# Kernel optimization log

Measured on AMD Instinct MI355X. Metric: run time of the kernel, lower is better.

## Reference

```python
import jax, jax.numpy as jnp
from jax import lax
import numpy as np

B, N0 = 4, 4096
NIN, NH, NOUT = 16, 128, 2
DEPTH, K, RADIUS, KNN = 3, 64, 2.0, 3
EPS = 1e-5


def _bn(x, g, b):
    # eval-mode BatchNorm1d with running_mean=0, running_var=1
    return g * x / jnp.sqrt(1.0 + EPS) + b


def _mlp2(h, p):
    # Seq(Lin, ReLU, BN) x 2, as in MLP([d, d, out])
    w1, b1, g1, be1, w2, b2, g2, be2 = p
    h = _bn(jax.nn.relu(h @ w1 + b1), g1, be1)
    return _bn(jax.nn.relu(h @ w2 + b2), g2, be2)


def _fps(pts, m):
    # farthest point sampling, deterministic start at index 0
    n = pts.shape[0]
    def step(carry, _):
        dmin, last = carry
        d = jnp.sum((pts - pts[last]) ** 2, axis=-1)
        dmin = jnp.minimum(dmin, d)
        nxt = jnp.argmax(dmin).astype(jnp.int32)
        return (dmin, nxt), nxt
    _, rest = lax.scan(step, (jnp.full((n,), 1e30, pts.dtype), jnp.int32(0)), None, length=m - 1)
    return jnp.concatenate([jnp.zeros((1,), jnp.int32), rest])


def _sa(xx, pp, m, params):
    # SAModule with PointConv: fps -> radius(K nearest within r) -> gather-MLP-max
    idx = _fps(pp, m)
    q = pp[idx]                                              # [m,3] sampled centers
    d2 = jnp.sum((q[:, None, :] - pp[None, :, :]) ** 2, -1)  # [m,n]
    d2 = jnp.where(d2 <= RADIUS * RADIUS, d2, 1e30)
    neg, nbr = lax.top_k(-d2, K)                             # K nearest inside ball
    valid = neg > -1e29
    h = jnp.concatenate([xx[nbr], pp[nbr] - q[:, None, :]], axis=-1)  # [m,K,C+3]
    h = _mlp2(h, params)
    h = jnp.where(valid[..., None], h, -1e30)
    return jnp.max(h, axis=1), q                             # PointConv max aggr


def _fp(xx, pp, xs, ps, params):
    # FPModule: knn_interpolate (k=3, inverse squared-distance weights) + concat skip + MLP
    d2 = jnp.sum((ps[:, None, :] - pp[None, :, :]) ** 2, -1)  # [n_fine, n_coarse]
    neg, idx = lax.top_k(-d2, KNN)
    w = 1.0 / jnp.maximum(-neg, 1e-16)
    y = jnp.sum(w[..., None] * xx[idx], axis=1) / jnp.sum(w, axis=1, keepdims=True)
    return _mlp2(jnp.concatenate([y, xs], axis=-1), params)


def _forward(x, pos, lin_in_w, lin_in_b,
             sa_w1, sa_b1, sa_g1, sa_be1, sa_w2, sa_b2, sa_g2, sa_be2,
             fp_w1, fp_b1, fp_g1, fp_be1, fp_w2, fp_b2, fp_g2, fp_be2,
             lo_w1, lo_b1, lo_g1, lo_be1, lo_w2, lo_b2, lo_g2, lo_be2):
    xb = jax.nn.relu(x.reshape(B, N0, NIN) @ lin_in_w + lin_in_b)  # lin_in + ReLU
    posb = pos.reshape(B, N0, 3)
    sa = [(xb, posb)]
    n = N0
    for i in range(DEPTH):
        m = n // 2  # ratio = 0.5
        p = (sa_w1[i], sa_b1[i], sa_g1[i], sa_be1[i], sa_w2[i], sa_b2[i], sa_g2[i], sa_be2[i])
        h, q = jax.vmap(lambda a, b: _sa(a, b, m, p))(sa[i][0], sa[i][1])
        sa.append((h, q))
        n = m
    xf, posf = sa[DEPTH]
    for step in range(DEPTH):
        mi = DEPTH - 1 - step
        xs, ps = sa[DEPTH - 1 - step]
        p = (fp_w1[mi], fp_b1[mi], fp_g1[mi], fp_be1[mi], fp_w2[mi], fp_b2[mi], fp_g2[mi], fp_be2[mi])
        xf = jax.vmap(lambda a, b, c, d: _fp(a, b, c, d, p))(xf, posf, xs, ps)
        posf = ps
    out = _mlp2(xf, (lo_w1, lo_b1, lo_g1, lo_be1, lo_w2, lo_b2, lo_g2, lo_be2))
    return out.reshape(B * N0, NOUT)


def setup_inputs() -> dict:
    key = jax.random.key(0)
    ki = iter(jax.random.split(key, 24))
    def nrm(shape, s=0.1):
        return jax.random.normal(next(ki), shape, jnp.float32) * s
    D = NH + 3   # PointConv MLP in-dim
    F = 2 * NH   # FP MLP in-dim (nIn + nSkip)
    return {
        "x": jax.random.normal(next(ki), (B * N0, NIN), jnp.float32),
        "pos": jax.random.uniform(next(ki), (B * N0, 3), jnp.float32) * 16.0,
        "batch": jnp.repeat(jnp.arange(B, dtype=jnp.int32), N0),
        "lin_in_w": nrm((NIN, NH)), "lin_in_b": nrm((NH,)),
        "sa_w1": nrm((DEPTH, D, D)), "sa_b1": nrm((DEPTH, D)),
        "sa_g1": jnp.ones((DEPTH, D)), "sa_be1": jnp.zeros((DEPTH, D)),
        "sa_w2": nrm((DEPTH, D, NH)), "sa_b2": nrm((DEPTH, NH)),
        "sa_g2": jnp.ones((DEPTH, NH)), "sa_be2": jnp.zeros((DEPTH, NH)),
        "fp_w1": nrm((DEPTH, F, F)), "fp_b1": nrm((DEPTH, F)),
        "fp_g1": jnp.ones((DEPTH, F)), "fp_be1": jnp.zeros((DEPTH, F)),
        "fp_w2": nrm((DEPTH, F, NH)), "fp_b2": nrm((DEPTH, NH)),
        "fp_g2": jnp.ones((DEPTH, NH)), "fp_be2": jnp.zeros((DEPTH, NH)),
        "lo_w1": nrm((NH, NH)), "lo_b1": nrm((NH,)),
        "lo_g1": jnp.ones((NH,)), "lo_be1": jnp.zeros((NH,)),
        "lo_w2": nrm((NH, NOUT)), "lo_b2": nrm((NOUT,)),
        "lo_g2": jnp.ones((NOUT,)), "lo_be2": jnp.zeros((NOUT,)),
    }


def reference(x, pos, batch, lin_in_w, lin_in_b,
              sa_w1, sa_b1, sa_g1, sa_be1, sa_w2, sa_b2, sa_g2, sa_be2,
              fp_w1, fp_b1, fp_g1, fp_be1, fp_w2, fp_b2, fp_g2, fp_be2,
              lo_w1, lo_b1, lo_g1, lo_be1, lo_w2, lo_b2, lo_g2, lo_be2):
    return _forward(x, pos, lin_in_w, lin_in_b,
                    sa_w1, sa_b1, sa_g1, sa_be1, sa_w2, sa_b2, sa_g2, sa_be2,
                    fp_w1, fp_b1, fp_g1, fp_be1, fp_w2, fp_b2, fp_g2, fp_be2,
                    lo_w1, lo_b1, lo_g1, lo_be1, lo_w2, lo_b2, lo_g2, lo_be2)
```

## Files before the change

### kernel.cpp

```cpp
#include <hip/hip_runtime.h>
#include <cstddef>


#define EPSF 1e-5f

typedef __attribute__((ext_vector_type(2))) float f32x2;

__device__ __forceinline__ f32x2 f2splat(float s) {
    f32x2 v; v.x = s; v.y = s; return v;
}

__device__ __forceinline__ float d2_rn(float dx, float dy, float dz) {
    return __fadd_rn(__fadd_rn(__fmul_rn(dx, dx), __fmul_rn(dy, dy)), __fmul_rn(dz, dz));
}

template <int CTRL, int RMASK>
__device__ __forceinline__ float dpp_max_f32(float v) {
    int o = __builtin_amdgcn_update_dpp(__float_as_int(v), __float_as_int(v),
                                        CTRL, RMASK, 0xf, false);
    return fmaxf(v, __int_as_float(o));
}

template <int N, int NT>
__device__ void fps_role(const float* __restrict__ pts, float* __restrict__ q,
                         const int m, const int b, char* smem) {
#pragma clang fp contract(off)
    constexpr int PPT = N / NT;
    constexpr int PH = PPT / 2;
    constexpr int NW = NT / 64;
    float* s_px = (float*)smem;
    float* s_py = s_px + N;
    float* s_pz = s_py + N;
    int*   s_qi = (int*)(s_pz + N);
    float2* s_slot = (float2*)(s_qi + N / 2);
    const int t = threadIdx.x;
    const int wave = t >> 6, lane = t & 63;
    const int base = t * PPT;
    const float* P = pts + (size_t)b * N * 3;
    asm volatile("s_setprio 3");
    f32x2 rx[PH], ry[PH], rz[PH], dmin[PH];
#pragma unroll
    for (int j = 0; j < PH; ++j) {
        int i = base + 2 * j;
        float x0 = P[i * 3 + 0], y0 = P[i * 3 + 1], z0 = P[i * 3 + 2];
        float x1 = P[i * 3 + 3], y1 = P[i * 3 + 4], z1 = P[i * 3 + 5];
        rx[j].x = x0; rx[j].y = x1;
        ry[j].x = y0; ry[j].y = y1;
        rz[j].x = z0; rz[j].y = z1;
        dmin[j] = f2splat(1e30f);
        s_px[i] = x0; s_px[i + 1] = x1;
        s_py[i] = y0; s_py[i + 1] = y1;
        s_pz[i] = z0; s_pz[i + 1] = z1;
    }
    float lx = P[0], ly = P[1], lz = P[2];
    if (t == 0) s_qi[0] = 0;

    for (int step = 1; step < m; ++step) {
        float bv = -1.0f; int bj = 0;
        const f32x2 lxv = f2splat(lx), lyv = f2splat(ly), lzv = f2splat(lz);
#pragma unroll
        for (int j = 0; j < PH; ++j) {
            f32x2 dx = rx[j] - lxv;
            f32x2 dy = ry[j] - lyv;
            f32x2 dz = rz[j] - lzv;
            f32x2 d = dx * dx + dy * dy + dz * dz;
            float m0 = fminf(dmin[j].x, d.x);
            float m1 = fminf(dmin[j].y, d.y);
            dmin[j].x = m0; dmin[j].y = m1;
            if (m0 > bv) { bv = m0; bj = 2 * j; }
            if (m1 > bv) { bv = m1; bj = 2 * j + 1; }
        }
        const int bidx = base + bj;

        float v = bv;
        v = dpp_max_f32<0x111, 0xf>(v);
        v = dpp_max_f32<0x112, 0xf>(v);
        v = dpp_max_f32<0x114, 0xf>(v);
        v = dpp_max_f32<0x118, 0xf>(v);
        v = dpp_max_f32<0x142, 0xa>(v);
        v = dpp_max_f32<0x143, 0xc>(v);
        const float mv = __int_as_float(__builtin_amdgcn_readlane(__float_as_int(v), 63));
        unsigned long long mb = __ballot(bv == mv);
        const int wl = __ffsll((long long)mb) - 1;
        const int wbi = __builtin_amdgcn_readlane(bidx, wl);

        const int p = step & 1;
        if (lane == 0) s_slot[p * NW + wave] = make_float2(mv, __int_as_float(wbi));
        __syncthreads();

        float2 sl = s_slot[p * NW + (lane & (NW - 1))];
        float gvt = sl.x;
        gvt = dpp_max_f32<0x111, 0xf>(gvt);
        gvt = dpp_max_f32<0x112, 0xf>(gvt);
        if (NW == 8) gvt = dpp_max_f32<0x114, 0xf>(gvt);
        const float gm = __int_as_float(
            __builtin_amdgcn_readlane(__float_as_int(gvt), NW - 1));
        unsigned long long gb = __ballot((lane < NW) && (sl.x == gm));
        const int gl = __ffsll((long long)gb) - 1;
        const int gi = __builtin_amdgcn_readlane(__float_as_int(sl.y), gl);

        lx = s_px[gi]; ly = s_py[gi]; lz = s_pz[gi];
        if (t == 0) s_qi[step] = gi;
    }
    __syncthreads();
    for (int e = t; e < m; e += NT) {
        int gi = s_qi[e];
        size_t o = ((size_t)b * m + e) * 3;
        q[o] = s_px[gi]; q[o + 1] = s_py[gi]; q[o + 2] = s_pz[gi];
    }
}

__device__ void lin_role(const float* __restrict__ x, const float* __restrict__ w,
                         const float* __restrict__ bias, float* __restrict__ xb,
                         const int blk) {
    const int t = threadIdx.x;
    const int row = blk * 2 + (t >> 7);
    const int col = t & 127;
    float acc = bias[col];
#pragma unroll
    for (int k = 0; k < 16; ++k) acc = fmaf(x[row * 16 + k], w[k * 128 + col], acc);
    xb[row * 128 + col] = fmaxf(acc, 0.0f);
}

template <int CHUNK, int WACT>
__device__ void nbr_role(const float* __restrict__ pts, const float* __restrict__ q,
                         int2* __restrict__ pairs, unsigned* __restrict__ counter,
                         const int n, const int m, const int pstr, const int qstr,
                         const int blk, char* smem) {
    const int w = threadIdx.x >> 6, lane = threadIdx.x & 63;
    if (w >= WACT) return;
    float* D = (float*)smem + w * CHUNK * 64;
    const int c = blk * WACT + w;
    const int b = c / m;
    const int r = c - b * m;
    const float* P = pts + (size_t)b * pstr * 3;
    const size_t qo = ((size_t)b * qstr + r) * 3;
    const float qx = q[qo + 0];
    const float qy = q[qo + 1];
    const float qz = q[qo + 2];
    for (int s = 0; s < CHUNK; ++s) {
        int i = s * 64 + lane;
        float d2 = d2_rn(P[i * 3] - qx, P[i * 3 + 1] - qy, P[i * 3 + 2] - qz);
        D[i] = (d2 <= 4.0f) ? d2 : 1e30f;
    }
    int my_g = -1;
    int cnt = 0;
    for (int round = 0; round < 64; ++round) {
        float bv = 3e38f;
        int bi = 0x7fffffff;
        for (int s = 0; s < CHUNK; ++s) {
            int i = s * 64 + lane;
            float v = D[i];
            if (v < bv) { bv = v; bi = i; }
        }
#pragma unroll
        for (int off = 32; off >= 1; off >>= 1) {
            float ov = __shfl_xor(bv, off, 64);
            int   oi = __shfl_xor(bi, off, 64);
            if (ov < bv || (ov == bv && oi < bi)) { bv = ov; bi = oi; }
        }
        if (bv > 1e29f) break;
        if (round == lane) my_g = bi;
        if (lane == (bi & 63)) D[bi] = 3e38f;
        ++cnt;
    }
    unsigned base = 0;
    if (lane == 0) base = atomicAdd(counter, (unsigned)cnt);
    base = (unsigned)__shfl((int)base, 0, 64);
    if (lane < cnt) pairs[base + lane] = make_int2(c, my_g);
}

typedef float Row132[132];
__device__ void sa_body(const float* __restrict__ xx, const float* __restrict__ ptsc,
    const float* __restrict__ qc, const int2* __restrict__ pairs,
    const unsigned* __restrict__ vcount,
    const float* __restrict__ wp1, const float* __restrict__ b1,
    const float* __restrict__ g1, const float* __restrict__ be1,
    const float* __restrict__ wp2, const float* __restrict__ b2,
    const float* __restrict__ g2, const float* __restrict__ be2,
    float* __restrict__ hout, const int lm, const int ln, const int lnp,
    const int blk, char* smem) {
    Row132* shA = (Row132*)smem;
    int* sh_c = (int*)(smem + 33792);
    int* sh_g = sh_c + 64;
    const int t = threadIdx.x;
    const int V = (int)*vcount;
    const int r0 = blk * 64;
    if (r0 >= V) return;
    if (t < 64) {
        int r = r0 + t;
        if (r < V) { int2 p = pairs[r]; sh_c[t] = p.x; sh_g[t] = p.y; }
        else { sh_c[t] = -1; sh_g[t] = 0; }
    }
    __syncthreads();

    for (int e = t; e < 64 * 33; e += 256) {
        int row = e / 33, cid = e - row * 33;
        int c = sh_c[row];
        float4 v = make_float4(0.f, 0.f, 0.f, 0.f);
        if (c >= 0) {
            int g = sh_g[row];
            int b = c >> lm;
            if (cid < 32) {
                size_t ptf = ((size_t)(b << ln) + g);
                v = *(const float4*)(xx + (ptf << 7) + cid * 4);
            } else {
                size_t ptc = ((size_t)(b << lnp) + g);
                const float* P = ptsc + ptc * 3;
                int r = c - (b << lm);
                const float* Q = qc + ((size_t)((b << 11) + r)) * 3;
                v.x = P[0] - Q[0]; v.y = P[1] - Q[1]; v.z = P[2] - Q[2]; v.w = 0.f;
            }
        }
        *(float4*)&shA[row][cid * 4] = v;
    }
    __syncthreads();

    const float invs = 1.0f / sqrtf(1.0f + EPSF);
    const int tr = t >> 4, tc = t & 15;
    const int xrow = t >> 2, xcol = t & 3;
    float acc[32];
#pragma unroll
    for (int i = 0; i < 32; ++i) acc[i] = 0.0f;
    float accx = 0.0f;

    for (int k = 0; k < 132; k += 4) {
        const float4 A0 = *(const float4*)&shA[tr     ][k];
        const float4 A1 = *(const float4*)&shA[tr + 16][k];
        const float4 A2 = *(const float4*)&shA[tr + 32][k];
        const float4 A3 = *(const float4*)&shA[tr + 48][k];
        const float4 AX = *(const float4*)&shA[xrow][k];
        const float a0v[4] = {A0.x, A0.y, A0.z, A0.w};
        const float a1v[4] = {A1.x, A1.y, A1.z, A1.w};
        const float a2v[4] = {A2.x, A2.y, A2.z, A2.w};
        const float a3v[4] = {A3.x, A3.y, A3.z, A3.w};
        const float axv[4] = {AX.x, AX.y, AX.z, AX.w};
#pragma unroll
        for (int u = 0; u < 4; ++u) {
            const float* wr = wp1 + (size_t)(k + u) * 132;
            const float4 w0 = *(const float4*)(wr + 8 * tc);
            const float4 w1v = *(const float4*)(wr + 8 * tc + 4);
            const float wx = wr[128 + xcol];
            const float wa[8] = {w0.x, w0.y, w0.z, w0.w, w1v.x, w1v.y, w1v.z, w1v.w};
#pragma unroll
            for (int j = 0; j < 8; ++j) {
                acc[0 * 8 + j] = fmaf(a0v[u], wa[j], acc[0 * 8 + j]);
                acc[1 * 8 + j] = fmaf(a1v[u], wa[j], acc[1 * 8 + j]);
                acc[2 * 8 + j] = fmaf(a2v[u], wa[j], acc[2 * 8 + j]);
                acc[3 * 8 + j] = fmaf(a3v[u], wa[j], acc[3 * 8 + j]);
            }
            accx = fmaf(axv[u], wx, accx);
        }
    }
    __syncthreads();
#pragma unroll
    for (int i = 0; i < 4; ++i)
#pragma unroll
        for (int j = 0; j < 8; ++j) {
            int col = 8 * tc + j;
            float z = fmaxf(acc[i * 8 + j] + b1[col], 0.0f);
            shA[tr + 16 * i][col] = g1[col] * z * invs + be1[col];
        }
    if (xcol < 3) {
        int col = 128 + xcol;
        float z = fmaxf(accx + b1[col], 0.0f);
        shA[xrow][col] = g1[col] * z * invs + be1[col];
    } else {
        shA[xrow][131] = 0.0f;
    }
    __syncthreads();

#pragma unroll
    for (int i = 0; i < 32; ++i) acc[i] = 0.0f;
    for (int k = 0; k < 132; k += 4) {
        const float4 A0 = *(const float4*)&shA[tr     ][k];
        const float4 A1 = *(const float4*)&shA[tr + 16][k];
        const float4 A2 = *(const float4*)&shA[tr + 32][k];
        const float4 A3 = *(const float4*)&shA[tr + 48][k];
        const float a0v[4] = {A0.x, A0.y, A0.z, A0.w};
        const float a1v[4] = {A1.x, A1.y, A1.z, A1.w};
        const float a2v[4] = {A2.x, A2.y, A2.z, A2.w};
        const float a3v[4] = {A3.x, A3.y, A3.z, A3.w};
#pragma unroll
        for (int u = 0; u < 4; ++u) {
            const float* wr = wp2 + (size_t)(k + u) * 128;
            const float4 w0 = *(const float4*)(wr + 8 * tc);
            const float4 w1v = *(const float4*)(wr + 8 * tc + 4);
            const float wa[8] = {w0.x, w0.y, w0.z, w0.w, w1v.x, w1v.y, w1v.z, w1v.w};
#pragma unroll
            for (int j = 0; j < 8; ++j) {
                acc[0 * 8 + j] = fmaf(a0v[u], wa[j], acc[0 * 8 + j]);
                acc[1 * 8 + j] = fmaf(a1v[u], wa[j], acc[1 * 8 + j]);
                acc[2 * 8 + j] = fmaf(a2v[u], wa[j], acc[2 * 8 + j]);
                acc[3 * 8 + j] = fmaf(a3v[u], wa[j], acc[3 * 8 + j]);
            }
        }
    }
    __syncthreads();
#pragma unroll
    for (int i = 0; i < 4; ++i)
#pragma unroll
        for (int j = 0; j < 8; ++j) {
            int col = 8 * tc + j;
            float z = fmaxf(acc[i * 8 + j] + b2[col], 0.0f);
            shA[tr + 16 * i][col] = g2[col] * z * invs + be2[col];
        }
    __syncthreads();

    if (t < 128) {
        const int col = t;
        float run = -1.0f;
        int cur = sh_c[0];
        for (int row = 0; row < 64; ++row) {
            int c = sh_c[row];
            if (c != cur) {
                if (cur >= 0)
                    atomicMax((unsigned*)&hout[((size_t)cur << 7) + col], __float_as_uint(run));
                run = -1.0f; cur = c;
            }
            run = fmaxf(run, shA[row][col]);
        }
        if (cur >= 0)
            atomicMax((unsigned*)&hout[((size_t)cur << 7) + col], __float_as_uint(run));
    }
}

__device__ void knn_role(const float* __restrict__ pf, const float* __restrict__ pc,
                         int* __restrict__ kidx, float* __restrict__ kw,
                         const int nf, const int nc, const int fstr, const int cstr,
                         const int blk) {
    const int tg = blk * 256 + threadIdx.x;
    const int b = tg / nf;
    const int rf = tg - b * nf;
    const float* F = pf + ((size_t)b * fstr + rf) * 3;
    const float fx = F[0], fy = F[1], fz = F[2];
    const float* C = pc + (size_t)b * cstr * 3;
    float b0 = 1e30f, b1 = 1e30f, b2 = 1e30f;
    int i0 = 0, i1 = 0, i2 = 0;
    for (int j = 0; j < nc; ++j) {
        float d2 = d2_rn(C[j * 3] - fx, C[j * 3 + 1] - fy, C[j * 3 + 2] - fz);
        if (d2 < b0)      { b2 = b1; i2 = i1; b1 = b0; i1 = i0; b0 = d2; i0 = j; }
        else if (d2 < b1) { b2 = b1; i2 = i1; b1 = d2; i1 = j; }
        else if (d2 < b2) { b2 = d2; i2 = j; }
    }
    float w0 = 1.0f / fmaxf(b0, 1e-16f);
    float w1 = 1.0f / fmaxf(b1, 1e-16f);
    float w2 = 1.0f / fmaxf(b2, 1e-16f);
    float inv = 1.0f / (w0 + w1 + w2);
    size_t o = (size_t)tg * 3;
    kidx[o] = i0; kidx[o + 1] = i1; kidx[o + 2] = i2;
    kw[o] = w0 * inv; kw[o + 1] = w1 * inv; kw[o + 2] = w2 * inv;
}

__global__ __launch_bounds__(256) void stage_a_kernel(
    const float* __restrict__ pos, float* __restrict__ q1,
    const float* __restrict__ x, const float* __restrict__ lin_w,
    const float* __restrict__ lin_b, float* __restrict__ xb,
    float* __restrict__ hbuf, unsigned* __restrict__ ctrs,
    const float* __restrict__ sa_w1, const float* __restrict__ sa_w2,
    float* __restrict__ wp1, float* __restrict__ wp2) {
    __shared__ __align__(16) char smem[57408];
    const int blk = blockIdx.x;
    if (blk < 4) {
        fps_role<4096, 256>(pos, q1, 2048, blk, smem);
    } else if (blk < 4 + 8192) {
        lin_role(x, lin_w, lin_b, xb, blk - 4);
    } else if (blk < 4 + 8192 + 1792) {
        const int i = blk - 8196;
        *(float4*)(hbuf + (size_t)i * 1024 + threadIdx.x * 4) =
            make_float4(0.f, 0.f, 0.f, 0.f);
        if (i == 0 && threadIdx.x < 3) ctrs[threadIdx.x * 16] = 0u;
    } else {
        const int f = (blk - 9988) * 256 + threadIdx.x;
        if (f < 52272) {
            int col = f % 132; int r = f / 132;
            int k = r % 132; int lvl = r / 132;
            float v = 0.0f;
            if (k < 131 && col < 131)
                v = sa_w1[(size_t)lvl * 131 * 131 + k * 131 + col];
            wp1[f] = v;
        } else if (f < 52272 + 50688) {
            int f2 = f - 52272;
            int col = f2 & 127; int r = f2 >> 7;
            int k = r % 132; int lvl = r / 132;
            float v = 0.0f;
            if (k < 131)
                v = sa_w2[(size_t)lvl * 131 * 128 + k * 128 + col];
            wp2[f2] = v;
        }
    }
}

__global__ __launch_bounds__(256) void stage_b_kernel(
    const float* __restrict__ pos, const float* __restrict__ q1,
    int2* __restrict__ pairs1, unsigned* __restrict__ ctr0,
    int2* __restrict__ pairs2, unsigned* __restrict__ ctr1,
    int2* __restrict__ pairs3, unsigned* __restrict__ ctr2,
    int* __restrict__ kidx2, float* __restrict__ kw2,
    int* __restrict__ kidx1, float* __restrict__ kw1,
    int* __restrict__ kidx0, float* __restrict__ kw0) {
    __shared__ __align__(16) char smem[32768];
    const int blk = blockIdx.x;
    if (blk < 4096)
        nbr_role<64, 2>(pos, q1, pairs1, ctr0, 4096, 2048, 4096, 2048, blk, smem);
    else if (blk < 4096 + 1024)
        nbr_role<32, 4>(q1, q1, pairs2, ctr1, 2048, 1024, 2048, 2048, blk - 4096, smem);
    else if (blk < 4096 + 1024 + 512)
        nbr_role<16, 4>(q1, q1, pairs3, ctr2, 1024, 512, 2048, 2048, blk - 5120, smem);
    else if (blk < 5632 + 64)
        knn_role(pos, q1, kidx2, kw2, 4096, 2048, 4096, 2048, blk - 5632);
    else if (blk < 5696 + 32)
        knn_role(q1, q1, kidx1, kw1, 2048, 1024, 2048, 2048, blk - 5696);
    else
        knn_role(q1, q1, kidx0, kw0, 1024, 512, 2048, 2048, blk - 5728);
}

__global__ __launch_bounds__(256) void sa_fused_kernel(
    const float* xx, const float* ptsc, const float* qc, const int2* pairs,
    const unsigned* vcount,
    const float* wp1, const float* b1, const float* g1, const float* be1,
    const float* wp2, const float* b2, const float* g2, const float* be2,
    float* hout, int lm, int ln, int lnp) {
    __shared__ __align__(16) char smem[34304];
    sa_body(xx, ptsc, qc, pairs, vcount, wp1, b1, g1, be1, wp2, b2, g2, be2,
            hout, lm, ln, lnp, blockIdx.x, smem);
}

__global__ __launch_bounds__(256) void fp_fused_kernel(
    const float* __restrict__ xc, const float* __restrict__ xs,
    const int* __restrict__ kidx, const float* __restrict__ kw,
    const float* __restrict__ w1, const float* __restrict__ b1,
    const float* __restrict__ g1, const float* __restrict__ be1,
    const float* __restrict__ w2, const float* __restrict__ b2,
    const float* __restrict__ g2, const float* __restrict__ be2,
    float* __restrict__ out, int lnf) {
    __shared__ __align__(16) float shA[32][260];
    const int t = threadIdx.x;
    const int r0 = blockIdx.x * 32;
    const float invs = 1.0f / sqrtf(1.0f + EPSF);

    for (int e = t; e < 32 * 64; e += 256) {
        int r = e >> 6, cid = e & 63;
        int fr = r0 + r;
        float4 v;
        if (cid < 32) {
            int b = fr >> lnf;
            size_t o = (size_t)fr * 3;
            int i0 = kidx[o], i1 = kidx[o + 1], i2 = kidx[o + 2];
            float u0 = kw[o], u1 = kw[o + 1], u2 = kw[o + 2];
            const float* X = xc + (((size_t)b << lnf) >> 1) * 128;
            const float4 A0 = *(const float4*)(X + (size_t)i0 * 128 + cid * 4);
            const float4 A1 = *(const float4*)(X + (size_t)i1 * 128 + cid * 4);
            const float4 A2 = *(const float4*)(X + (size_t)i2 * 128 + cid * 4);
            v.x = u0 * A0.x + u1 * A1.x + u2 * A2.x;
            v.y = u0 * A0.y + u1 * A1.y + u2 * A2.y;
            v.z = u0 * A0.z + u1 * A1.z + u2 * A2.z;
            v.w = u0 * A0.w + u1 * A1.w + u2 * A2.w;
        } else {
            v = *(const float4*)(xs + (size_t)fr * 128 + (cid - 32) * 4);
        }
        *(float4*)&shA[r][cid * 4] = v;
    }
    __syncthreads();

    const int tr = t >> 5, tc = t & 31;
    float acc[32];
#pragma unroll
    for (int i = 0; i < 32; ++i) acc[i] = 0.0f;
    for (int k = 0; k < 256; k += 4) {
        const float4 A0 = *(const float4*)&shA[tr     ][k];
        const float4 A1 = *(const float4*)&shA[tr +  8][k];
        const float4 A2 = *(const float4*)&shA[tr + 16][k];
        const float4 A3 = *(const float4*)&shA[tr + 24][k];
        const float a0v[4] = {A0.x, A0.y, A0.z, A0.w};
        const float a1v[4] = {A1.x, A1.y, A1.z, A1.w};
        const float a2v[4] = {A2.x, A2.y, A2.z, A2.w};
        const float a3v[4] = {A3.x, A3.y, A3.z, A3.w};
#pragma unroll
        for (int u = 0; u < 4; ++u) {
            const float* wr = w1 + (size_t)(k + u) * 256;
            const float4 w0v = *(const float4*)(wr + 8 * tc);
            const float4 w1v = *(const float4*)(wr + 8 * tc + 4);
            const float wa[8] = {w0v.x, w0v.y, w0v.z, w0v.w, w1v.x, w1v.y, w1v.z, w1v.w};
#pragma unroll
            for (int j = 0; j < 8; ++j) {
                acc[0 * 8 + j] = fmaf(a0v[u], wa[j], acc[0 * 8 + j]);
                acc[1 * 8 + j] = fmaf(a1v[u], wa[j], acc[1 * 8 + j]);
                acc[2 * 8 + j] = fmaf(a2v[u], wa[j], acc[2 * 8 + j]);
                acc[3 * 8 + j] = fmaf(a3v[u], wa[j], acc[3 * 8 + j]);
            }
        }
    }
    __syncthreads();
#pragma unroll
    for (int i = 0; i < 4; ++i)
#pragma unroll
        for (int j = 0; j < 8; ++j) {
            int col = 8 * tc + j;
            float z = fmaxf(acc[i * 8 + j] + b1[col], 0.0f);
            shA[tr + 8 * i][col] = g1[col] * z * invs + be1[col];
        }
    __syncthreads();

    const int tr2 = t >> 4, tc2 = t & 15;
    float acc2[16];
#pragma unroll
    for (int i = 0; i < 16; ++i) acc2[i] = 0.0f;
    for (int k = 0; k < 256; k += 4) {
        const float4 A0 = *(const float4*)&shA[tr2     ][k];
        const float4 A1 = *(const float4*)&shA[tr2 + 16][k];
        const float a0v[4] = {A0.x, A0.y, A0.z, A0.w};
        const float a1v[4] = {A1.x, A1.y, A1.z, A1.w};
#pragma unroll
        for (int u = 0; u < 4; ++u) {
            const float* wr = w2 + (size_t)(k + u) * 128;
            const float4 w0v = *(const float4*)(wr + 8 * tc2);
            const float4 w1v = *(const float4*)(wr + 8 * tc2 + 4);
            const float wa[8] = {w0v.x, w0v.y, w0v.z, w0v.w, w1v.x, w1v.y, w1v.z, w1v.w};
#pragma unroll
            for (int j = 0; j < 8; ++j) {
                acc2[0 * 8 + j] = fmaf(a0v[u], wa[j], acc2[0 * 8 + j]);
                acc2[1 * 8 + j] = fmaf(a1v[u], wa[j], acc2[1 * 8 + j]);
            }
        }
    }
#pragma unroll
    for (int i = 0; i < 2; ++i)
#pragma unroll
        for (int j = 0; j < 8; ++j) {
            int col = 8 * tc2 + j;
            int fr = r0 + tr2 + 16 * i;
            float z = fmaxf(acc2[i * 8 + j] + b2[col], 0.0f);
            out[(size_t)fr * 128 + col] = g2[col] * z * invs + be2[col];
        }
}

__global__ __launch_bounds__(256) void lo_fused_kernel(
    const float* __restrict__ in,
    const float* __restrict__ w1, const float* __restrict__ b1,
    const float* __restrict__ g1, const float* __restrict__ be1,
    const float* __restrict__ w2, const float* __restrict__ b2,
    const float* __restrict__ g2, const float* __restrict__ be2,
    float* __restrict__ out) {
    __shared__ __align__(16) float shA[32][132];
    const int t = threadIdx.x;
    const int r0 = blockIdx.x * 32;
    const float invs = 1.0f / sqrtf(1.0f + EPSF);

    for (int e = t; e < 32 * 32; e += 256) {
        int r = e >> 5, cid = e & 31;
        *(float4*)&shA[r][cid * 4] =
            *(const float4*)(in + (size_t)(r0 + r) * 128 + cid * 4);
    }
    __syncthreads();

    const int tr = t >> 4, tc = t & 15;
    float acc[16];
#pragma unroll
    for (int i = 0; i < 16; ++i) acc[i] = 0.0f;
    for (int k = 0; k < 128; k += 4) {
        const float4 A0 = *(const float4*)&shA[2 * tr + 0][k];
        const float4 A1 = *(const float4*)&shA[2 * tr + 1][k];
        const float a0v[4] = {A0.x, A0.y, A0.z, A0.w};
        const float a1v[4] = {A1.x, A1.y, A1.z, A1.w};
#pragma unroll
        for (int u = 0; u < 4; ++u) {
            const float* wr = w1 + (size_t)(k + u) * 128;
            const float4 w0v = *(const float4*)(wr + 8 * tc);
            const float4 w1v = *(const float4*)(wr + 8 * tc + 4);
            const float wa[8] = {w0v.x, w0v.y, w0v.z, w0v.w, w1v.x, w1v.y, w1v.z, w1v.w};
#pragma unroll
            for (int j = 0; j < 8; ++j) {
                acc[0 * 8 + j] = fmaf(a0v[u], wa[j], acc[0 * 8 + j]);
                acc[1 * 8 + j] = fmaf(a1v[u], wa[j], acc[1 * 8 + j]);
            }
        }
    }
    __syncthreads();
#pragma unroll
    for (int i = 0; i < 2; ++i)
#pragma unroll
        for (int j = 0; j < 8; ++j) {
            int col = 8 * tc + j;
            float z = fmaxf(acc[i * 8 + j] + b1[col], 0.0f);
            shA[2 * tr + i][col] = g1[col] * z * invs + be1[col];
        }
    __syncthreads();

    if (t < 64) {
        const int row = t >> 1, col = t & 1;
        float a = b2[col];
        for (int k = 0; k < 128; ++k)
            a = fmaf(shA[row][k], w2[k * 2 + col], a);
        a = fmaxf(a, 0.0f);
        out[(size_t)(r0 + row) * 2 + col] = g2[col] * a * invs + be2[col];
    }
}

extern "C" void kernel_launch(void* const* d_in, const int* in_sizes, int n_in,
                              void* d_out, int out_size, void* d_ws, size_t ws_size,
                              hipStream_t stream) {
    const float* x      = (const float*)d_in[0];
    const float* pos    = (const float*)d_in[1];
    const float* lin_w  = (const float*)d_in[3];
    const float* lin_b  = (const float*)d_in[4];
    const float* sa_w1  = (const float*)d_in[5];
    const float* sa_b1  = (const float*)d_in[6];
    const float* sa_g1  = (const float*)d_in[7];
    const float* sa_be1 = (const float*)d_in[8];
    const float* sa_w2  = (const float*)d_in[9];
    const float* sa_b2  = (const float*)d_in[10];
    const float* sa_g2  = (const float*)d_in[11];
    const float* sa_be2 = (const float*)d_in[12];
    const float* fp_w1  = (const float*)d_in[13];
    const float* fp_b1  = (const float*)d_in[14];
    const float* fp_g1  = (const float*)d_in[15];
    const float* fp_be1 = (const float*)d_in[16];
    const float* fp_w2  = (const float*)d_in[17];
    const float* fp_b2  = (const float*)d_in[18];
    const float* fp_g2  = (const float*)d_in[19];
    const float* fp_be2 = (const float*)d_in[20];
    const float* lo_w1  = (const float*)d_in[21];
    const float* lo_b1  = (const float*)d_in[22];
    const float* lo_g1  = (const float*)d_in[23];
    const float* lo_be1 = (const float*)d_in[24];
    const float* lo_w2  = (const float*)d_in[25];
    const float* lo_b2  = (const float*)d_in[26];
    const float* lo_g2  = (const float*)d_in[27];
    const float* lo_be2 = (const float*)d_in[28];

    float* ws = (float*)d_ws;
    size_t off = 0;
    auto alloc = [&](size_t n) { float* p = ws + off; off += n; return p; };
    float* xb    = alloc(4 * 4096 * 128);
    float* q1    = alloc(4 * 2048 * 3);
    float* h1    = alloc(4 * 2048 * 128);
    float* h2    = alloc(4 * 1024 * 128);
    float* h3    = alloc(4 * 512 * 128);
    int2* pairs1 = (int2*)alloc(4 * 2048 * 64 * 2);
    int2* pairs2 = (int2*)alloc(4 * 1024 * 64 * 2);
    int2* pairs3 = (int2*)alloc(4 * 512 * 64 * 2);
    unsigned* ctrs = (unsigned*)alloc(64);
    int* kidx0   = (int*)alloc(4 * 1024 * 3);
    float* kw0   = alloc(4 * 1024 * 3);
    int* kidx1   = (int*)alloc(4 * 2048 * 3);
    float* kw1   = alloc(4 * 2048 * 3);
    int* kidx2   = (int*)alloc(4 * 4096 * 3);
    float* kw2   = alloc(4 * 4096 * 3);
    float* xfA   = alloc(4 * 4096 * 128);
    float* xfB   = alloc(4 * 4096 * 128);
    float* wp1   = alloc(3 * 132 * 132);
    float* wp2   = alloc(3 * 132 * 128);
    if (ws_size < off * sizeof(float)) return;

    stage_a_kernel<<<4 + 8192 + 1792 + 403, 256, 0, stream>>>(
        pos, q1, x, lin_w, lin_b, xb, h1, ctrs, sa_w1, sa_w2, wp1, wp2);

    stage_b_kernel<<<4096 + 1024 + 512 + 64 + 32 + 16, 256, 0, stream>>>(
        pos, q1, pairs1, ctrs + 0, pairs2, ctrs + 16, pairs3, ctrs + 32,
        kidx2, kw2, kidx1, kw1, kidx0, kw0);

    sa_fused_kernel<<<8192, 256, 0, stream>>>(xb, pos, q1, pairs1, ctrs + 0,
        wp1, sa_b1, sa_g1, sa_be1, wp2, sa_b2, sa_g2, sa_be2,
        h1, 11, 12, 12);

    sa_fused_kernel<<<4096, 256, 0, stream>>>(h1, q1, q1, pairs2, ctrs + 16,
        wp1 + 132 * 132, sa_b1 + 131, sa_g1 + 131, sa_be1 + 131,
        wp2 + 132 * 128, sa_b2 + 128, sa_g2 + 128, sa_be2 + 128,
        h2, 10, 11, 11);

    sa_fused_kernel<<<2048, 256, 0, stream>>>(h2, q1, q1, pairs3, ctrs + 32,
        wp1 + 2 * 132 * 132, sa_b1 + 2 * 131, sa_g1 + 2 * 131, sa_be1 + 2 * 131,
        wp2 + 2 * 132 * 128, sa_b2 + 2 * 128, sa_g2 + 2 * 128, sa_be2 + 2 * 128,
        h3, 9, 10, 11);

    fp_fused_kernel<<<4 * 1024 / 32, 256, 0, stream>>>(h3, h2, kidx0, kw0,
        fp_w1 + 2 * 256 * 256, fp_b1 + 2 * 256, fp_g1 + 2 * 256, fp_be1 + 2 * 256,
        fp_w2 + 2 * 256 * 128, fp_b2 + 2 * 128, fp_g2 + 2 * 128, fp_be2 + 2 * 128,
        xfA, 10);

    fp_fused_kernel<<<4 * 2048 / 32, 256, 0, stream>>>(xfA, h1, kidx1, kw1,
        fp_w1 + 256 * 256, fp_b1 + 256, fp_g1 + 256, fp_be1 + 256,
        fp_w2 + 256 * 128, fp_b2 + 128, fp_g2 + 128, fp_be2 + 128,
        xfB, 11);

    fp_fused_kernel<<<4 * 4096 / 32, 256, 0, stream>>>(xfB, xb, kidx2, kw2,
        fp_w1, fp_b1, fp_g1, fp_be1, fp_w2, fp_b2, fp_g2, fp_be2,
        xfA, 12);

    lo_fused_kernel<<<16384 / 32, 256, 0, stream>>>(xfA,
        lo_w1, lo_b1, lo_g1, lo_be1, lo_w2, lo_b2, lo_g2, lo_be2,
        (float*)d_out);
}
```

Baseline: 2.699 ms.

## Remap SA MLP GEMM to per-wave column slices with wave-uniform weights

The SA fused kernel's two-layer MLP now gives each wave a contiguous slice of output columns (33 or 32) and each lane one gathered row, so weight reads are wave-uniform and can be broadcast or scalarised. Before, each thread computed a 4x8 tile and read per-lane weight vectors from global memory. The packed weight buffers are re-laid out per wave (36- and 32-wide slices) in the stage-A prep role to match. The cost is that every lane reads its own shared-memory row, which may cause bank conflicts, and it needs 33 accumulators with less register reuse of A.

Result: slower. 3.659 ms (+35.6%).

```diff
diff --git a/kernel.cpp b/kernel.cpp
--- a/kernel.cpp
+++ b/kernel.cpp
@@ -217,95 +217,88 @@
     __syncthreads();
 
     const float invs = 1.0f / sqrtf(1.0f + EPSF);
-    const int tr = t >> 4, tc = t & 15;
-    const int xrow = t >> 2, xcol = t & 3;
-    float acc[32];
-#pragma unroll
-    for (int i = 0; i < 32; ++i) acc[i] = 0.0f;
-    float accx = 0.0f;
-
-    for (int k = 0; k < 132; k += 4) {
-        const float4 A0 = *(const float4*)&shA[tr     ][k];
-        const float4 A1 = *(const float4*)&shA[tr + 16][k];
-        const float4 A2 = *(const float4*)&shA[tr + 32][k];
-        const float4 A3 = *(const float4*)&shA[tr + 48][k];
-        const float4 AX = *(const float4*)&shA[xrow][k];
-        const float a0v[4] = {A0.x, A0.y, A0.z, A0.w};
-        const float a1v[4] = {A1.x, A1.y, A1.z, A1.w};
-        const float a2v[4] = {A2.x, A2.y, A2.z, A2.w};
-        const float a3v[4] = {A3.x, A3.y, A3.z, A3.w};
-        const float axv[4] = {AX.x, AX.y, AX.z, AX.w};
-#pragma unroll
-        for (int u = 0; u < 4; ++u) {
-            const float* wr = wp1 + (size_t)(k + u) * 132;
-            const float4 w0 = *(const float4*)(wr + 8 * tc);
-            const float4 w1v = *(const float4*)(wr + 8 * tc + 4);
-            const float wx = wr[128 + xcol];
-            const float wa[8] = {w0.x, w0.y, w0.z, w0.w, w1v.x, w1v.y, w1v.z, w1v.w};
-#pragma unroll
-            for (int j = 0; j < 8; ++j) {
-                acc[0 * 8 + j] = fmaf(a0v[u], wa[j], acc[0 * 8 + j]);
-                acc[1 * 8 + j] = fmaf(a1v[u], wa[j], acc[1 * 8 + j]);
-                acc[2 * 8 + j] = fmaf(a2v[u], wa[j], acc[2 * 8 + j]);
-                acc[3 * 8 + j] = fmaf(a3v[u], wa[j], acc[3 * 8 + j]);
-            }
-            accx = fmaf(axv[u], wx, accx);
-        }
-    }
-    __syncthreads();
-#pragma unroll
-    for (int i = 0; i < 4; ++i)
-#pragma unroll
-        for (int j = 0; j < 8; ++j) {
-            int col = 8 * tc + j;
-            float z = fmaxf(acc[i * 8 + j] + b1[col], 0.0f);
-            shA[tr + 16 * i][col] = g1[col] * z * invs + be1[col];
-        }
-    if (xcol < 3) {
-        int col = 128 + xcol;
-        float z = fmaxf(accx + b1[col], 0.0f);
-        shA[xrow][col] = g1[col] * z * invs + be1[col];
-    } else {
-        shA[xrow][131] = 0.0f;
-    }
-    __syncthreads();
-
-#pragma unroll
-    for (int i = 0; i < 32; ++i) acc[i] = 0.0f;
-    for (int k = 0; k < 132; k += 4) {
-        const float4 A0 = *(const float4*)&shA[tr     ][k];
-        const float4 A1 = *(const float4*)&shA[tr + 16][k];
-        const float4 A2 = *(const float4*)&shA[tr + 32][k];
-        const float4 A3 = *(const float4*)&shA[tr + 48][k];
-        const float a0v[4] = {A0.x, A0.y, A0.z, A0.w};
-        const float a1v[4] = {A1.x, A1.y, A1.z, A1.w};
-        const float a2v[4] = {A2.x, A2.y, A2.z, A2.w};
-        const float a3v[4] = {A3.x, A3.y, A3.z, A3.w};
-#pragma unroll
-        for (int u = 0; u < 4; ++u) {
-            const float* wr = wp2 + (size_t)(k + u) * 128;
-            const float4 w0 = *(const float4*)(wr + 8 * tc);
-            const float4 w1v = *(const float4*)(wr + 8 * tc + 4);
-            const float wa[8] = {w0.x, w0.y, w0.z, w0.w, w1v.x, w1v.y, w1v.z, w1v.w};
-#pragma unroll
-            for (int j = 0; j < 8; ++j) {
-                acc[0 * 8 + j] = fmaf(a0v[u], wa[j], acc[0 * 8 + j]);
-                acc[1 * 8 + j] = fmaf(a1v[u], wa[j], acc[1 * 8 + j]);
-                acc[2 * 8 + j] = fmaf(a2v[u], wa[j], acc[2 * 8 + j]);
-                acc[3 * 8 + j] = fmaf(a3v[u], wa[j], acc[3 * 8 + j]);
-            }
-        }
-    }
-    __syncthreads();
-#pragma unroll
-    for (int i = 0; i < 4; ++i)
-#pragma unroll
-        for (int j = 0; j < 8; ++j) {
-            int col = 8 * tc + j;
-            float z = fmaxf(acc[i * 8 + j] + b2[col], 0.0f);
-            shA[tr + 16 * i][col] = g2[col] * z * invs + be2[col];
-        }
-    __syncthreads();
+    const int wave = t >> 6, lane = t & 63;
+
+    {
+        const float* W = wp1 + (size_t)wave * (132 * 36);
+        float acc[33];
+#pragma unroll
+        for (int i = 0; i < 33; ++i) acc[i] = 0.0f;
+        for (int k = 0; k < 132; k += 4) {
+            const float4 A4 = *(const float4*)&shA[lane][k];
+            const float av[4] = {A4.x, A4.y, A4.z, A4.w};
+#pragma unroll
+            for (int u = 0; u < 4; ++u) {
+                const float* wr = W + (size_t)(k + u) * 36;
+                const float4 q0 = *(const float4*)(wr + 0);
+                const float4 q1v = *(const float4*)(wr + 4);
+                const float4 q2v = *(const float4*)(wr + 8);
+                const float4 q3v = *(const float4*)(wr + 12);
+                const float4 q4 = *(const float4*)(wr + 16);
+                const float4 q5 = *(const float4*)(wr + 20);
+                const float4 q6 = *(const float4*)(wr + 24);
+                const float4 q7 = *(const float4*)(wr + 28);
+                const float wlast = wr[32];
+                const float wv[33] = {q0.x, q0.y, q0.z, q0.w, q1v.x, q1v.y, q1v.z, q1v.w,
+                                      q2v.x, q2v.y, q2v.z, q2v.w, q3v.x, q3v.y, q3v.z, q3v.w,
+                                      q4.x, q4.y, q4.z, q4.w, q5.x, q5.y, q5.z, q5.w,
+                                      q6.x, q6.y, q6.z, q6.w, q7.x, q7.y, q7.z, q7.w, wlast};
+#pragma unroll
+                for (int c = 0; c < 33; ++c)
+                    acc[c] = fmaf(av[u], wv[c], acc[c]);
+            }
+        }
+        __syncthreads();
+#pragma unroll
+        for (int c = 0; c < 33; ++c) {
+            int col = 33 * wave + c;
+            if (col < 131) {
+                float z = fmaxf(acc[c] + b1[col], 0.0f);
+                shA[lane][col] = g1[col] * z * invs + be1[col];
+            } else if (col == 131) {
+                shA[lane][131] = 0.0f;
+            }
+        }
+        __syncthreads();
+    }
+
+    {
+        const float* W = wp2 + (size_t)wave * (132 * 32);
+        float acc[32];
+#pragma unroll
+        for (int i = 0; i < 32; ++i) acc[i] = 0.0f;
+        for (int k = 0; k < 132; k += 4) {
+            const float4 A4 = *(const float4*)&shA[lane][k];
+            const float av[4] = {A4.x, A4.y, A4.z, A4.w};
+#pragma unroll
+            for (int u = 0; u < 4; ++u) {
+                const float* wr = W + (size_t)(k + u) * 32;
+                const float4 q0 = *(const float4*)(wr + 0);
+                const float4 q1v = *(const float4*)(wr + 4);
+                const float4 q2v = *(const float4*)(wr + 8);
+                const float4 q3v = *(const float4*)(wr + 12);
+                const float4 q4 = *(const float4*)(wr + 16);
+                const float4 q5 = *(const float4*)(wr + 20);
+                const float4 q6 = *(const float4*)(wr + 24);
+                const float4 q7 = *(const float4*)(wr + 28);
+                const float wv[32] = {q0.x, q0.y, q0.z, q0.w, q1v.x, q1v.y, q1v.z, q1v.w,
+                                      q2v.x, q2v.y, q2v.z, q2v.w, q3v.x, q3v.y, q3v.z, q3v.w,
+                                      q4.x, q4.y, q4.z, q4.w, q5.x, q5.y, q5.z, q5.w,
+                                      q6.x, q6.y, q6.z, q6.w, q7.x, q7.y, q7.z, q7.w};
+#pragma unroll
+                for (int c = 0; c < 32; ++c)
+                    acc[c] = fmaf(av[u], wv[c], acc[c]);
+            }
+        }
+        __syncthreads();
+#pragma unroll
+        for (int c = 0; c < 32; ++c) {
+            int col = 32 * wave + c;
+            float z = fmaxf(acc[c] + b2[col], 0.0f);
+            shA[lane][col] = g2[col] * z * invs + be2[col];
+        }
+        __syncthreads();
+    }
 
     if (t < 128) {
         const int col = t;
@@ -372,20 +365,23 @@
         if (i == 0 && threadIdx.x < 3) ctrs[threadIdx.x * 16] = 0u;
     } else {
         const int f = (blk - 9988) * 256 + threadIdx.x;
-        if (f < 52272) {
-            int col = f % 132; int r = f / 132;
-            int k = r % 132; int lvl = r / 132;
+        if (f < 57024) {
+            int c = f % 36; int r = f / 36;
+            int k = r % 132; int s = r / 132;
+            int w = s & 3; int lvl = s >> 2;
+            int col = 33 * w + c;
             float v = 0.0f;
-            if (k < 131 && col < 131)
+            if (k < 131 && c < 33 && col < 131)
                 v = sa_w1[(size_t)lvl * 131 * 131 + k * 131 + col];
             wp1[f] = v;
-        } else if (f < 52272 + 50688) {
-            int f2 = f - 52272;
-            int col = f2 & 127; int r = f2 >> 7;
-            int k = r % 132; int lvl = r / 132;
+        } else if (f < 57024 + 50688) {
+            int f2 = f - 57024;
+            int c = f2 & 31; int r = f2 >> 5;
+            int k = r % 132; int s = r / 132;
+            int w = s & 3; int lvl = s >> 2;
             float v = 0.0f;
             if (k < 131)
-                v = sa_w2[(size_t)lvl * 131 * 128 + k * 128 + col];
+                v = sa_w2[(size_t)lvl * 131 * 128 + k * 128 + 32 * w + c];
             wp2[f2] = v;
         }
     }
@@ -649,11 +645,11 @@
     float* kw2   = alloc(4 * 4096 * 3);
     float* xfA   = alloc(4 * 4096 * 128);
     float* xfB   = alloc(4 * 4096 * 128);
-    float* wp1   = alloc(3 * 132 * 132);
-    float* wp2   = alloc(3 * 132 * 128);
+    float* wp1   = alloc(3 * 4 * 132 * 36);
+    float* wp2   = alloc(3 * 4 * 132 * 32);
     if (ws_size < off * sizeof(float)) return;
 
-    stage_a_kernel<<<4 + 8192 + 1792 + 403, 256, 0, stream>>>(
+    stage_a_kernel<<<4 + 8192 + 1792 + 421, 256, 0, stream>>>(
         pos, q1, x, lin_w, lin_b, xb, h1, ctrs, sa_w1, sa_w2, wp1, wp2);
 
     stage_b_kernel<<<4096 + 1024 + 512 + 64 + 32 + 16, 256, 0, stream>>>(
@@ -665,13 +661,13 @@
         h1, 11, 12, 12);
 
     sa_fused_kernel<<<4096, 256, 0, stream>>>(h1, q1, q1, pairs2, ctrs + 16,
-        wp1 + 132 * 132, sa_b1 + 131, sa_g1 + 131, sa_be1 + 131,
-        wp2 + 132 * 128, sa_b2 + 128, sa_g2 + 128, sa_be2 + 128,
+        wp1 + 4 * 132 * 36, sa_b1 + 131, sa_g1 + 131, sa_be1 + 131,
+        wp2 + 4 * 132 * 32, sa_b2 + 128, sa_g2 + 128, sa_be2 + 128,
         h2, 10, 11, 11);
 
     sa_fused_kernel<<<2048, 256, 0, stream>>>(h2, q1, q1, pairs3, ctrs + 32,
-        wp1 + 2 * 132 * 132, sa_b1 + 2 * 131, sa_g1 + 2 * 131, sa_be1 + 2 * 131,
-        wp2 + 2 * 132 * 128, sa_b2 + 2 * 128, sa_g2 + 2 * 128, sa_be2 + 2 * 128,
+        wp1 + 2 * 4 * 132 * 36, sa_b1 + 2 * 131, sa_g1 + 2 * 131, sa_be1 + 2 * 131,
+        wp2 + 2 * 4 * 132 * 32, sa_b2 + 2 * 128, sa_g2 + 2 * 128, sa_be2 + 2 * 128,
         h3, 9, 10, 11);
 
     fp_fused_kernel<<<4 * 1024 / 32, 256, 0, stream>>>(h3, h2, kidx0, kw0,
```

## Fuse FPS and neighbor-search stages with progress-flag streaming between blocks

Applied to the files above, without the earlier changes.

Stage A and stage B are merged into one launch. FPS blocks publish per-batch progress counters every 32 sampled points, and the neighbor/knn blocks spin-wait on those counters, so ball queries start while FPS is still running. FPS now writes centers directly instead of doing a final copy loop, and the counters are zeroed with a memset. This removes the kernel boundary serialization, but it relies on the FPS blocks being scheduled before the waiting blocks and adds spin-wait overhead. Blocks needing the full point set (levels 2/3 and knn) still wait for most of FPS to finish.

After: 2.846 ms. +5.4%, slower.

```diff
diff --git a/kernel.cpp b/kernel.cpp
--- a/kernel.cpp
+++ b/kernel.cpp
@@ -12,6 +12,11 @@
 
 __device__ __forceinline__ float d2_rn(float dx, float dy, float dz) {
     return __fadd_rn(__fadd_rn(__fmul_rn(dx, dx), __fmul_rn(dy, dy)), __fmul_rn(dz, dz));
+}
+
+__device__ __forceinline__ void wait_prog(const unsigned* p, unsigned need) {
+    while (__hip_atomic_load(p, __ATOMIC_ACQUIRE, __HIP_MEMORY_SCOPE_AGENT) < need)
+        __builtin_amdgcn_s_sleep(2);
 }
 
 template <int CTRL, int RMASK>
@@ -23,7 +28,8 @@
 
 template <int N, int NT>
 __device__ void fps_role(const float* __restrict__ pts, float* __restrict__ q,
-                         const int m, const int b, char* smem) {
+                         const int m, const int b, char* smem,
+                         unsigned* __restrict__ prog) {
 #pragma clang fp contract(off)
     constexpr int PPT = N / NT;
     constexpr int PH = PPT / 2;
@@ -53,7 +59,10 @@
         s_pz[i] = z0; s_pz[i + 1] = z1;
     }
     float lx = P[0], ly = P[1], lz = P[2];
-    if (t == 0) s_qi[0] = 0;
+    if (t == 0) {
+        size_t o = (size_t)b * m * 3;
+        q[o] = lx; q[o + 1] = ly; q[o + 2] = lz;
+    }
 
     for (int step = 1; step < m; ++step) {
         float bv = -1.0f; int bj = 0;
@@ -100,13 +109,15 @@
         const int gi = __builtin_amdgcn_readlane(__float_as_int(sl.y), gl);
 
         lx = s_px[gi]; ly = s_py[gi]; lz = s_pz[gi];
-        if (t == 0) s_qi[step] = gi;
-    }
-    __syncthreads();
-    for (int e = t; e < m; e += NT) {
-        int gi = s_qi[e];
-        size_t o = ((size_t)b * m + e) * 3;
-        q[o] = s_px[gi]; q[o + 1] = s_py[gi]; q[o + 2] = s_pz[gi];
+        if (t == 0) {
+            size_t o = ((size_t)b * m + step) * 3;
+            q[o] = lx; q[o + 1] = ly; q[o + 2] = lz;
+            if ((step & 31) == 31 || step == m - 1) {
+                __threadfence();
+                __hip_atomic_store(prog + b, (unsigned)(step + 1),
+                                   __ATOMIC_RELEASE, __HIP_MEMORY_SCOPE_AGENT);
+            }
+        }
     }
 }
 
@@ -126,13 +137,16 @@
 __device__ void nbr_role(const float* __restrict__ pts, const float* __restrict__ q,
                          int2* __restrict__ pairs, unsigned* __restrict__ counter,
                          const int n, const int m, const int pstr, const int qstr,
-                         const int blk, char* smem) {
+                         const int blk, char* smem,
+                         const unsigned* __restrict__ prog, const int wait_pts) {
     const int w = threadIdx.x >> 6, lane = threadIdx.x & 63;
     if (w >= WACT) return;
     float* D = (float*)smem + w * CHUNK * 64;
     const int c = blk * WACT + w;
     const int b = c / m;
     const int r = c - b * m;
+    const int needi = (wait_pts > r + 1) ? wait_pts : (r + 1);
+    wait_prog(prog + b, (unsigned)needi);
     const float* P = pts + (size_t)b * pstr * 3;
     const size_t qo = ((size_t)b * qstr + r) * 3;
     const float qx = q[qo + 0];
@@ -328,10 +342,13 @@
 __device__ void knn_role(const float* __restrict__ pf, const float* __restrict__ pc,
                          int* __restrict__ kidx, float* __restrict__ kw,
                          const int nf, const int nc, const int fstr, const int cstr,
-                         const int blk) {
+                         const int blk, const unsigned* __restrict__ prog,
+                         const int cneed, const int fq1) {
     const int tg = blk * 256 + threadIdx.x;
     const int b = tg / nf;
     const int rf = tg - b * nf;
+    const int needi = fq1 ? ((rf + 1 > cneed) ? rf + 1 : cneed) : cneed;
+    wait_prog(prog + b, (unsigned)needi);
     const float* F = pf + ((size_t)b * fstr + rf) * 3;
     const float fx = F[0], fy = F[1], fz = F[2];
     const float* C = pc + (size_t)b * cstr * 3;
@@ -352,25 +369,30 @@
     kw[o] = w0 * inv; kw[o + 1] = w1 * inv; kw[o + 2] = w2 * inv;
 }
 
-__global__ __launch_bounds__(256) void stage_a_kernel(
+__global__ __launch_bounds__(256) void stage_ab_kernel(
     const float* __restrict__ pos, float* __restrict__ q1,
     const float* __restrict__ x, const float* __restrict__ lin_w,
     const float* __restrict__ lin_b, float* __restrict__ xb,
     float* __restrict__ hbuf, unsigned* __restrict__ ctrs,
     const float* __restrict__ sa_w1, const float* __restrict__ sa_w2,
-    float* __restrict__ wp1, float* __restrict__ wp2) {
+    float* __restrict__ wp1, float* __restrict__ wp2,
+    int2* __restrict__ pairs1, int2* __restrict__ pairs2,
+    int2* __restrict__ pairs3,
+    int* __restrict__ kidx2, float* __restrict__ kw2,
+    int* __restrict__ kidx1, float* __restrict__ kw1,
+    int* __restrict__ kidx0, float* __restrict__ kw0) {
     __shared__ __align__(16) char smem[57408];
+    unsigned* prog = ctrs + 48;
     const int blk = blockIdx.x;
     if (blk < 4) {
-        fps_role<4096, 256>(pos, q1, 2048, blk, smem);
+        fps_role<4096, 256>(pos, q1, 2048, blk, smem, prog);
     } else if (blk < 4 + 8192) {
         lin_role(x, lin_w, lin_b, xb, blk - 4);
     } else if (blk < 4 + 8192 + 1792) {
         const int i = blk - 8196;
         *(float4*)(hbuf + (size_t)i * 1024 + threadIdx.x * 4) =
             make_float4(0.f, 0.f, 0.f, 0.f);
-        if (i == 0 && threadIdx.x < 3) ctrs[threadIdx.x * 16] = 0u;
-    } else {
+    } else if (blk < 10391) {
         const int f = (blk - 9988) * 256 + threadIdx.x;
         if (f < 52272) {
             int col = f % 132; int r = f / 132;
@@ -388,31 +410,25 @@
                 v = sa_w2[(size_t)lvl * 131 * 128 + k * 128 + col];
             wp2[f2] = v;
         }
-    }
-}
-
-__global__ __launch_bounds__(256) void stage_b_kernel(
-    const float* __restrict__ pos, const float* __restrict__ q1,
-    int2* __restrict__ pairs1, unsigned* __restrict__ ctr0,
-    int2* __restrict__ pairs2, unsigned* __restrict__ ctr1,
-    int2* __restrict__ pairs3, unsigned* __restrict__ ctr2,
-    int* __restrict__ kidx2, float* __restrict__ kw2,
-    int* __restrict__ kidx1, float* __restrict__ kw1,
-    int* __restrict__ kidx0, float* __restrict__ kw0) {
-    __shared__ __align__(16) char smem[32768];
-    const int blk = blockIdx.x;
-    if (blk < 4096)
-        nbr_role<64, 2>(pos, q1, pairs1, ctr0, 4096, 2048, 4096, 2048, blk, smem);
-    else if (blk < 4096 + 1024)
-        nbr_role<32, 4>(q1, q1, pairs2, ctr1, 2048, 1024, 2048, 2048, blk - 4096, smem);
-    else if (blk < 4096 + 1024 + 512)
-        nbr_role<16, 4>(q1, q1, pairs3, ctr2, 1024, 512, 2048, 2048, blk - 5120, smem);
-    else if (blk < 5632 + 64)
-        knn_role(pos, q1, kidx2, kw2, 4096, 2048, 4096, 2048, blk - 5632);
-    else if (blk < 5696 + 32)
-        knn_role(q1, q1, kidx1, kw1, 2048, 1024, 2048, 2048, blk - 5696);
-    else
-        knn_role(q1, q1, kidx0, kw0, 1024, 512, 2048, 2048, blk - 5728);
+    } else if (blk < 10391 + 4096) {
+        nbr_role<64, 2>(pos, q1, pairs1, ctrs + 0, 4096, 2048, 4096, 2048,
+                        blk - 10391, smem, prog, 0);
+    } else if (blk < 14487 + 1024) {
+        nbr_role<32, 4>(q1, q1, pairs2, ctrs + 16, 2048, 1024, 2048, 2048,
+                        blk - 14487, smem, prog, 2048);
+    } else if (blk < 15511 + 512) {
+        nbr_role<16, 4>(q1, q1, pairs3, ctrs + 32, 1024, 512, 2048, 2048,
+                        blk - 15511, smem, prog, 1024);
+    } else if (blk < 16023 + 64) {
+        knn_role(pos, q1, kidx2, kw2, 4096, 2048, 4096, 2048,
+                 blk - 16023, prog, 2048, 0);
+    } else if (blk < 16087 + 32) {
+        knn_role(q1, q1, kidx1, kw1, 2048, 1024, 2048, 2048,
+                 blk - 16087, prog, 1024, 1);
+    } else {
+        knn_role(q1, q1, kidx0, kw0, 1024, 512, 2048, 2048,
+                 blk - 16119, prog, 512, 1);
+    }
 }
 
 __global__ __launch_bounds__(256) void sa_fused_kernel(
@@ -653,12 +669,11 @@
     float* wp2   = alloc(3 * 132 * 128);
     if (ws_size < off * sizeof(float)) return;
 
-    stage_a_kernel<<<4 + 8192 + 1792 + 403, 256, 0, stream>>>(
-        pos, q1, x, lin_w, lin_b, xb, h1, ctrs, sa_w1, sa_w2, wp1, wp2);
-
-    stage_b_kernel<<<4096 + 1024 + 512 + 64 + 32 + 16, 256, 0, stream>>>(
-        pos, q1, pairs1, ctrs + 0, pairs2, ctrs + 16, pairs3, ctrs + 32,
-        kidx2, kw2, kidx1, kw1, kidx0, kw0);
+    hipMemsetAsync((void*)ctrs, 0, 64 * sizeof(unsigned), stream);
+
+    stage_ab_kernel<<<16135, 256, 0, stream>>>(
+        pos, q1, x, lin_w, lin_b, xb, h1, ctrs, sa_w1, sa_w2, wp1, wp2,
+        pairs1, pairs2, pairs3, kidx2, kw2, kidx1, kw1, kidx0, kw0);
 
     sa_fused_kernel<<<8192, 256, 0, stream>>>(xb, pos, q1, pairs1, ctrs + 0,
         wp1, sa_b1, sa_g1, sa_be1, wp2, sa_b2, sa_g2, sa_be2,
```
